# Kernel optimization log

Hardware: AMD Instinct MI355X
Metric: run time of the kernel (lower is better)

The kernel has to match this reference:

```python
import jax, jax.numpy as jnp
import numpy as np
import math

EMBED_DIM = 1024
NUM_HEADS = 16
HEAD_DIM = EMBED_DIM // NUM_HEADS
MAX_LEN = 5000
LN_EPS = 1e-5


def _positional_encoding(max_len, embed_dim):
    pos = np.arange(max_len, dtype=np.float32)[:, None]
    div = np.exp(np.arange(0, embed_dim, 2, dtype=np.float32) * (-math.log(10000.0) / embed_dim))
    pe = np.zeros((max_len, embed_dim), dtype=np.float32)
    pe[:, 0::2] = np.sin(pos * div)
    pe[:, 1::2] = np.cos(pos * div)
    return jnp.asarray(pe)[None]  # [1, max_len, D]


def setup_inputs() -> dict:
    key = jax.random.key(0)
    ks = jax.random.split(key, 12)
    s = 1.0 / math.sqrt(EMBED_DIM)
    D = EMBED_DIM
    return {
        "x": jax.random.normal(ks[0], (4, 2048, D), dtype=jnp.float32),
        "wq": jax.random.uniform(ks[1], (D, D), jnp.float32, -s, s),
        "bq": jax.random.uniform(ks[2], (D,), jnp.float32, -s, s),
        "wk": jax.random.uniform(ks[3], (D, D), jnp.float32, -s, s),
        "bk": jax.random.uniform(ks[4], (D,), jnp.float32, -s, s),
        "wv": jax.random.uniform(ks[5], (D, D), jnp.float32, -s, s),
        "bv": jax.random.uniform(ks[6], (D,), jnp.float32, -s, s),
        "wo": jax.random.uniform(ks[7], (D, D), jnp.float32, -s, s),
        "bo": jax.random.uniform(ks[8], (D,), jnp.float32, -s, s),
        "gamma": jnp.ones((D,), jnp.float32),
        "beta": jnp.zeros((D,), jnp.float32),
        "pe": _positional_encoding(MAX_LEN, D),
    }


def reference(x, wq, bq, wk, bk, wv, bv, wo, bo, gamma, beta, pe):
    B, S, D = x.shape
    H, Hd = NUM_HEADS, HEAD_DIM
    x = x + pe[:, :S, :]
    # projections; weights stored as [in, out]
    q = (x @ wq + bq).reshape(B, S, H, Hd).transpose(0, 2, 1, 3)
    k = (x @ wk + bk).reshape(B, S, H, Hd).transpose(0, 2, 1, 3)
    v = (x @ wv + bv).reshape(B, S, H, Hd).transpose(0, 2, 1, 3)
    scores = jnp.einsum("bhqd,bhkd->bhqk", q, k) / math.sqrt(Hd)
    attn = jax.nn.softmax(scores, axis=-1)  # dropout is identity in eval
    out = jnp.einsum("bhqk,bhkd->bhqd", attn, v)
    out = out.transpose(0, 2, 1, 3).reshape(B, S, D)
    out = out @ wo + bo
    # residual + layernorm
    h = out + x
    mu = jnp.mean(h, axis=-1, keepdims=True)
    var = jnp.var(h, axis=-1, keepdims=True)
    return (h - mu) * jax.lax.rsqrt(var + LN_EPS) * gamma + beta
```

## Files before the change

kernel.cpp:

```cpp
#include <hip/hip_runtime.h>

#define DEV __device__ __forceinline__

typedef __attribute__((ext_vector_type(4))) float floatx4;
typedef __attribute__((ext_vector_type(8))) short short8;

DEV unsigned short f2bf(float f) {
  unsigned u = __float_as_uint(f);
  u += 0x7FFF + ((u >> 16) & 1);
  return (unsigned short)(u >> 16);
}
DEV float bf2f(unsigned short h) { return __uint_as_float(((unsigned)h) << 16); }

DEV unsigned pkbf(float lo, float hi) {
  return __builtin_amdgcn_perm(__float_as_uint(hi) + 0x8000u,
                               __float_as_uint(lo) + 0x8000u, 0x07060302u);
}

#if __has_builtin(__builtin_amdgcn_exp2f)
#define EXP2(x) __builtin_amdgcn_exp2f(x)
#else
#define EXP2(x) exp2f(x)
#endif

#define GLD16(g, l)                                                            \
  __builtin_amdgcn_global_load_lds(                                            \
      (const __attribute__((address_space(1))) void*)(g),                      \
      (__attribute__((address_space(3))) void*)(l), 16, 0, 0)

__global__ void k_wt(const float* __restrict__ w0, const float* __restrict__ w1,
                     const float* __restrict__ w2, const float* __restrict__ w3,
                     unsigned short* __restrict__ wt) {
  __shared__ float t[64][65];
  const float* wsel = (blockIdx.z == 0) ? w0
                    : (blockIdx.z == 1) ? w1
                    : (blockIdx.z == 2) ? w2 : w3;
  unsigned short* out = wt + (size_t)blockIdx.z * 1024 * 1024;
  const int tx = threadIdx.x, ty = threadIdx.y;
  const int k0 = blockIdx.x * 64, n0 = blockIdx.y * 64;
  for (int i = ty; i < 64; i += 4)
    t[i][tx] = wsel[(size_t)(k0 + i) * 1024 + n0 + tx];
  __syncthreads();
  for (int i = ty; i < 64; i += 4)
    out[(size_t)(n0 + i) * 1024 + k0 + tx] = f2bf(t[tx][i]);
}

__global__ void k_addpe(const float* __restrict__ x, const float* __restrict__ pe,
                        float* __restrict__ xf, unsigned short* __restrict__ xb) {
  const int idx = blockIdx.x * 256 + threadIdx.x;
  const int row = idx >> 8;
  const int c4 = idx & 255;
  const int s = row & 2047;
  const float4 xv = ((const float4*)x)[idx];
  const float4 pv = ((const float4*)pe)[s * 256 + c4];
  float4 r;
  r.x = xv.x + pv.x; r.y = xv.y + pv.y; r.z = xv.z + pv.z; r.w = xv.w + pv.w;
  ((float4*)xf)[idx] = r;
  ushort4 o;
  o.x = f2bf(r.x); o.y = f2bf(r.y); o.z = f2bf(r.z); o.w = f2bf(r.w);
  ((ushort4*)xb)[idx] = o;
}

__global__ __launch_bounds__(256) void k_gemmqkv(
    const unsigned short* __restrict__ A, const unsigned short* __restrict__ Bt,
    const float* __restrict__ bqp, const float* __restrict__ bkp,
    const float* __restrict__ bvp, unsigned short* __restrict__ qb,
    unsigned short* __restrict__ kb, unsigned short* __restrict__ vtb) {
  __shared__ unsigned short As[128 * 32];
  __shared__ unsigned short Bs[128 * 32];
  const int tid = threadIdx.x;
  const int lane = tid & 63, wave = tid >> 6;
  const int quad = lane >> 4, l16 = lane & 15;
  const int wm = wave >> 1, wn = wave & 1;
  const int rb = blockIdx.x * 128, cb = blockIdx.y * 128;
  const int which = cb >> 10;
  const float* bias = (which == 0) ? bqp : (which == 1) ? bkp : bvp;
  unsigned short* out = (which == 0) ? qb : (which == 1) ? kb : vtb;

  floatx4 acc[4][4];
  const floatx4 vzero = {0.f, 0.f, 0.f, 0.f};
#pragma unroll
  for (int i = 0; i < 4; ++i)
#pragma unroll
    for (int j = 0; j < 4; ++j) acc[i][j] = vzero;

  for (int k0 = 0; k0 < 1024; k0 += 32) {
#pragma unroll
    for (int r = 0; r < 2; ++r) {
      const int c = r * 256 + tid;
      const int arow = c >> 2, koff = (c & 3) << 3;
      GLD16(A + (size_t)(rb + arow) * 1024 + k0 + koff,
            As + (size_t)(r * 256 + wave * 64) * 8);
      GLD16(Bt + (size_t)(cb + arow) * 1024 + k0 + koff,
            Bs + (size_t)(r * 256 + wave * 64) * 8);
    }
    __syncthreads();
    short8 fa[4], fb[4];
#pragma unroll
    for (int i = 0; i < 4; ++i) {
      fa[i] = *(const short8*)(As + (wm * 64 + i * 16 + l16) * 32 + quad * 8);
      fb[i] = *(const short8*)(Bs + (wn * 64 + i * 16 + l16) * 32 + quad * 8);
    }
#pragma unroll
    for (int mi = 0; mi < 4; ++mi)
#pragma unroll
      for (int ni = 0; ni < 4; ++ni)
        acc[mi][ni] =
            __builtin_amdgcn_mfma_f32_16x16x32_bf16(fa[mi], fb[ni], acc[mi][ni], 0, 0, 0);
    __syncthreads();
  }

#pragma unroll
  for (int ni = 0; ni < 4; ++ni) {
    const int col = cb + wn * 64 + ni * 16 + l16;
    const int cl = col & 1023;
    const float bvv = bias[cl];
    const int h = cl >> 6, d = cl & 63;
#pragma unroll
    for (int mi = 0; mi < 4; ++mi) {
#pragma unroll
      for (int r = 0; r < 4; ++r) {
        const int row = rb + wm * 64 + mi * 16 + quad * 4 + r;
        const int b = row >> 11, s = row & 2047;
        const float val = acc[mi][ni][r] + bvv;
        if (which < 2) {
          out[((size_t)(b * 16 + h) * 2048 + s) * 64 + d] = f2bf(val);
        } else {
          out[((size_t)(b * 16 + h) * 64 + d) * 2048 + s] = f2bf(val);
        }
      }
    }
  }
}

__global__ __launch_bounds__(256) void k_gemmo(
    const unsigned short* __restrict__ A, const unsigned short* __restrict__ Bt,
    const float* __restrict__ bias, unsigned short* __restrict__ out) {
  __shared__ unsigned short As[128 * 32];
  __shared__ unsigned short Bs[128 * 32];
  const int tid = threadIdx.x;
  const int lane = tid & 63, wave = tid >> 6;
  const int quad = lane >> 4, l16 = lane & 15;
  const int wm = wave >> 1, wn = wave & 1;
  const int rb = blockIdx.x * 128, cb = blockIdx.y * 128;

  floatx4 acc[4][4];
  const floatx4 vzero = {0.f, 0.f, 0.f, 0.f};
#pragma unroll
  for (int i = 0; i < 4; ++i)
#pragma unroll
    for (int j = 0; j < 4; ++j) acc[i][j] = vzero;

  for (int k0 = 0; k0 < 1024; k0 += 32) {
#pragma unroll
    for (int r = 0; r < 2; ++r) {
      const int c = r * 256 + tid;
      const int arow = c >> 2, koff = (c & 3) << 3;
      GLD16(A + (size_t)(rb + arow) * 1024 + k0 + koff,
            As + (size_t)(r * 256 + wave * 64) * 8);
      GLD16(Bt + (size_t)(cb + arow) * 1024 + k0 + koff,
            Bs + (size_t)(r * 256 + wave * 64) * 8);
    }
    __syncthreads();
    short8 fa[4], fb[4];
#pragma unroll
    for (int i = 0; i < 4; ++i) {
      fa[i] = *(const short8*)(As + (wm * 64 + i * 16 + l16) * 32 + quad * 8);
      fb[i] = *(const short8*)(Bs + (wn * 64 + i * 16 + l16) * 32 + quad * 8);
    }
#pragma unroll
    for (int mi = 0; mi < 4; ++mi)
#pragma unroll
      for (int ni = 0; ni < 4; ++ni)
        acc[mi][ni] =
            __builtin_amdgcn_mfma_f32_16x16x32_bf16(fa[mi], fb[ni], acc[mi][ni], 0, 0, 0);
    __syncthreads();
  }

#pragma unroll
  for (int ni = 0; ni < 4; ++ni) {
    const int col = cb + wn * 64 + ni * 16 + l16;
    const float bvv = bias[col];
#pragma unroll
    for (int mi = 0; mi < 4; ++mi) {
#pragma unroll
      for (int r = 0; r < 4; ++r) {
        const int row = rb + wm * 64 + mi * 16 + quad * 4 + r;
        out[(size_t)row * 1024 + col] = f2bf(acc[mi][ni][r] + bvv);
      }
    }
  }
}

__global__ __launch_bounds__(256) void k_flash(
    const unsigned short* __restrict__ Q, const unsigned short* __restrict__ Kb,
    const unsigned short* __restrict__ Vt, unsigned short* __restrict__ AO) {
  __shared__ unsigned short Ks[2][64 * 64];
  __shared__ unsigned short Vs[2][64 * 64];
  __shared__ unsigned short Ps[4][32 * 72];
  const int tid = threadIdx.x, lane = tid & 63, wave = tid >> 6;
  const int quad = lane >> 4, l16 = lane & 15;
  const int g = blockIdx.x;
  const int li = g >> 3;
  const int bh = (g & 7) * 8 + (li >> 4);
  const int qt = li & 15;
  const int b = bh >> 4, h = bh & 15;

  const unsigned short* Kh = Kb + (size_t)bh * 2048 * 64;
  const unsigned short* Vh = Vt + (size_t)bh * 64 * 2048;

  const float LAMBDA = 0.125f * 1.4426950408889634f;
  short8 aq[2][2];
  {
    const unsigned short* Qb = Q + ((size_t)bh * 2048 + qt * 128 + wave * 32) * 64;
#pragma unroll
    for (int qi = 0; qi < 2; ++qi)
#pragma unroll
      for (int c = 0; c < 2; ++c) {
        const short8 raw =
            *(const short8*)(Qb + (size_t)(qi * 16 + l16) * 64 + c * 32 + quad * 8);
        short8 sv;
#pragma unroll
        for (int j = 0; j < 8; ++j)
          sv[j] = (short)f2bf(bf2f((unsigned short)raw[j]) * LAMBDA);
        aq[qi][c] = sv;
      }
  }

  const floatx4 vzero = {0.f, 0.f, 0.f, 0.f};
  floatx4 o[2][4];
#pragma unroll
  for (int qi = 0; qi < 2; ++qi)
#pragma unroll
    for (int di = 0; di < 4; ++di) o[qi][di] = vzero;
  float l_p[2] = {0.f, 0.f};
  unsigned short* Pw = Ps[wave];

#define STAGE(ktile, buf)                                                      \
  {                                                                            \
    _Pragma("unroll") for (int r = 0; r < 2; ++r) {                            \
      const int c = r * 256 + tid;                                             \
      const int rw = c >> 3;                                                   \
      const int gc = ((c & 7) ^ (rw & 7)) * 8;                                 \
      GLD16(Kh + (size_t)((ktile) * 64 + rw) * 64 + gc,                        \
            &Ks[buf][(size_t)(r * 256 + wave * 64) * 8]);                      \
      GLD16(Vh + (size_t)rw * 2048 + (ktile) * 64 + gc,                        \
            &Vs[buf][(size_t)(r * 256 + wave * 64) * 8]);                      \
    }                                                                          \
  }

  STAGE(0, 0);
  __syncthreads();

  for (int kt = 0; kt < 32; ++kt) {
    const int buf = kt & 1;
    if (kt + 1 < 32) STAGE(kt + 1, buf ^ 1);

    short8 fk[4][2];
#pragma unroll
    for (int ni = 0; ni < 4; ++ni)
#pragma unroll
      for (int c = 0; c < 2; ++c)
        fk[ni][c] = *(const short8*)(&Ks[buf][(ni * 16 + l16) * 64 +
                                              (((c * 4 + quad) ^ (l16 & 7)) << 3)]);

#pragma unroll
    for (int qi = 0; qi < 2; ++qi) {
      floatx4 p[4];
#pragma unroll
      for (int ni = 0; ni < 4; ++ni) {
        floatx4 t = vzero;
#pragma unroll
        for (int c = 0; c < 2; ++c)
          t = __builtin_amdgcn_mfma_f32_16x16x32_bf16(fk[ni][c], aq[qi][c], t, 0, 0, 0);
        p[ni] = t;
      }
#pragma unroll
      for (int ni = 0; ni < 4; ++ni)
#pragma unroll
        for (int r = 0; r < 4; ++r) p[ni][r] = EXP2(p[ni][r]);
      const float s0 = (p[0][0] + p[0][1]) + (p[0][2] + p[0][3]);
      const float s1 = (p[1][0] + p[1][1]) + (p[1][2] + p[1][3]);
      const float s2 = (p[2][0] + p[2][1]) + (p[2][2] + p[2][3]);
      const float s3 = (p[3][0] + p[3][1]) + (p[3][2] + p[3][3]);
      l_p[qi] += (s0 + s1) + (s2 + s3);
#pragma unroll
      for (int ni = 0; ni < 4; ++ni) {
        uint2 pk;
        pk.x = pkbf(p[ni][0], p[ni][1]);
        pk.y = pkbf(p[ni][2], p[ni][3]);
        *(uint2*)(&Pw[(qi * 16 + l16) * 72 + ni * 16 + quad * 4]) = pk;
      }
    }
    asm volatile("s_waitcnt lgkmcnt(0)" ::: "memory");

#pragma unroll
    for (int c = 0; c < 2; ++c) {
      short8 ap[2];
#pragma unroll
      for (int qi = 0; qi < 2; ++qi)
        ap[qi] = *(const short8*)(&Pw[(qi * 16 + l16) * 72 + c * 32 + quad * 8]);
#pragma unroll
      for (int di = 0; di < 4; ++di) {
        const short8 fv = *(const short8*)(&Vs[buf][(di * 16 + l16) * 64 +
                                                    (((c * 4 + quad) ^ (l16 & 7)) << 3)]);
#pragma unroll
        for (int qi = 0; qi < 2; ++qi)
          o[qi][di] = __builtin_amdgcn_mfma_f32_16x16x32_bf16(ap[qi], fv, o[qi][di], 0, 0, 0);
      }
    }
    __syncthreads();
  }

  float* Al = (float*)Pw;
#pragma unroll
  for (int qi = 0; qi < 2; ++qi) {
    float l = l_p[qi];
    l += __shfl_xor(l, 16);
    l += __shfl_xor(l, 32);
    if (quad == 0) Al[qi * 16 + l16] = 1.0f / l;
  }
  asm volatile("s_waitcnt lgkmcnt(0)" ::: "memory");
#pragma unroll
  for (int qi = 0; qi < 2; ++qi) {
    const floatx4 invl = *(const floatx4*)(&Al[qi * 16 + quad * 4]);
#pragma unroll
    for (int di = 0; di < 4; ++di) {
#pragma unroll
      for (int r = 0; r < 4; ++r) {
        const int s = qt * 128 + wave * 32 + qi * 16 + quad * 4 + r;
        const int col = h * 64 + di * 16 + l16;
        AO[((size_t)b * 2048 + s) * 1024 + col] = f2bf(o[qi][di][r] * invl[r]);
      }
    }
  }
#undef STAGE
}

__global__ __launch_bounds__(256) void k_ln(
    const unsigned short* __restrict__ proj, const float* __restrict__ xpe,
    const float* __restrict__ gamma, const float* __restrict__ beta,
    float* __restrict__ out) {
  const int row = blockIdx.x, tid = threadIdx.x;
  const int lane = tid & 63, wave = tid >> 6;
  const float4 xv = ((const float4*)(xpe + (size_t)row * 1024))[tid];
  const ushort4 pv = ((const ushort4*)(proj + (size_t)row * 1024))[tid];
  const float h0 = xv.x + bf2f(pv.x);
  const float h1 = xv.y + bf2f(pv.y);
  const float h2 = xv.z + bf2f(pv.z);
  const float h3 = xv.w + bf2f(pv.w);
  float s = h0 + h1 + h2 + h3;
  float s2 = h0 * h0 + h1 * h1 + h2 * h2 + h3 * h3;
#pragma unroll
  for (int m = 1; m < 64; m <<= 1) {
    s += __shfl_xor(s, m);
    s2 += __shfl_xor(s2, m);
  }
  __shared__ float rs[4], rq[4];
  if (lane == 0) { rs[wave] = s; rq[wave] = s2; }
  __syncthreads();
  s = rs[0] + rs[1] + rs[2] + rs[3];
  s2 = rq[0] + rq[1] + rq[2] + rq[3];
  const float mu = s * (1.f / 1024.f);
  const float var = s2 * (1.f / 1024.f) - mu * mu;
  const float rstd = rsqrtf(var + 1e-5f);
  const float4 gv = ((const float4*)gamma)[tid];
  const float4 bvv = ((const float4*)beta)[tid];
  float4 ov;
  ov.x = (h0 - mu) * rstd * gv.x + bvv.x;
  ov.y = (h1 - mu) * rstd * gv.y + bvv.y;
  ov.z = (h2 - mu) * rstd * gv.z + bvv.z;
  ov.w = (h3 - mu) * rstd * gv.w + bvv.w;
  ((float4*)(out + (size_t)row * 1024))[tid] = ov;
}

extern "C" void kernel_launch(void* const* d_in, const int* in_sizes, int n_in,
                              void* d_out, int out_size, void* d_ws, size_t ws_size,
                              hipStream_t stream) {
  const float* x = (const float*)d_in[0];
  const float* wq = (const float*)d_in[1];
  const float* bq = (const float*)d_in[2];
  const float* wk = (const float*)d_in[3];
  const float* bk = (const float*)d_in[4];
  const float* wv = (const float*)d_in[5];
  const float* bv = (const float*)d_in[6];
  const float* wo = (const float*)d_in[7];
  const float* bo = (const float*)d_in[8];
  const float* gamma = (const float*)d_in[9];
  const float* beta = (const float*)d_in[10];
  const float* pe = (const float*)d_in[11];

  if (ws_size < 125829120) return;

  char* w = (char*)d_ws;
  unsigned short* wt = (unsigned short*)(w);
  float* xpef = (float*)(w + 8388608);
  unsigned short* xpeb = (unsigned short*)(w + 41943040);
  unsigned short* qb = (unsigned short*)(w + 58720256);
  unsigned short* kb = (unsigned short*)(w + 75497472);
  unsigned short* vtb = (unsigned short*)(w + 92274688);
  unsigned short* aob = (unsigned short*)(w + 109051904);
  unsigned short* projb = qb;

  k_wt<<<dim3(16, 16, 4), dim3(64, 4), 0, stream>>>(wq, wk, wv, wo, wt);
  k_addpe<<<8192, 256, 0, stream>>>(x, pe, xpef, xpeb);
  k_gemmqkv<<<dim3(64, 24), 256, 0, stream>>>(xpeb, wt, bq, bk, bv, qb, kb, vtb);
  k_flash<<<1024, 256, 0, stream>>>(qb, kb, vtb, aob);
  k_gemmo<<<dim3(64, 8), 256, 0, stream>>>(aob, wt + 3145728, bo, projb);
  k_ln<<<8192, 256, 0, stream>>>(projb, xpef, gamma, beta, (float*)d_out);
}
```

Baseline: 354.3 us.

## Split V projection into transposed GEMM, single-buffer flash tiles, MFMA row sums

The V projection moves into its own GEMM that computes W_v^T·X^T, so the transposed V output is written along contiguous sequence positions instead of with a 2048-element stride. The flash kernel drops K/V double buffering in favour of a single buffer with two barriers per tile and a launch bound of 4 blocks, trading load/compute overlap for lower LDS use and higher occupancy. The softmax denominator is now computed with an extra MFMA against a ones vector, using the bf16-rounded probabilities, which removes the scalar sums and the cross-lane reduction.

```diff
diff --git a/kernel.cpp b/kernel.cpp
--- a/kernel.cpp
+++ b/kernel.cpp
@@ -61,11 +61,10 @@
   ((ushort4*)xb)[idx] = o;
 }
 
-__global__ __launch_bounds__(256) void k_gemmqkv(
+__global__ __launch_bounds__(256) void k_gemmqk(
     const unsigned short* __restrict__ A, const unsigned short* __restrict__ Bt,
     const float* __restrict__ bqp, const float* __restrict__ bkp,
-    const float* __restrict__ bvp, unsigned short* __restrict__ qb,
-    unsigned short* __restrict__ kb, unsigned short* __restrict__ vtb) {
+    unsigned short* __restrict__ qb, unsigned short* __restrict__ kb) {
   __shared__ unsigned short As[128 * 32];
   __shared__ unsigned short Bs[128 * 32];
   const int tid = threadIdx.x;
@@ -74,8 +73,8 @@
   const int wm = wave >> 1, wn = wave & 1;
   const int rb = blockIdx.x * 128, cb = blockIdx.y * 128;
   const int which = cb >> 10;
-  const float* bias = (which == 0) ? bqp : (which == 1) ? bkp : bvp;
-  unsigned short* out = (which == 0) ? qb : (which == 1) ? kb : vtb;
+  const float* bias = (which == 0) ? bqp : bkp;
+  unsigned short* out = (which == 0) ? qb : kb;
 
   floatx4 acc[4][4];
   const floatx4 vzero = {0.f, 0.f, 0.f, 0.f};
@@ -122,12 +121,67 @@
       for (int r = 0; r < 4; ++r) {
         const int row = rb + wm * 64 + mi * 16 + quad * 4 + r;
         const int b = row >> 11, s = row & 2047;
-        const float val = acc[mi][ni][r] + bvv;
-        if (which < 2) {
-          out[((size_t)(b * 16 + h) * 2048 + s) * 64 + d] = f2bf(val);
-        } else {
-          out[((size_t)(b * 16 + h) * 64 + d) * 2048 + s] = f2bf(val);
-        }
+        out[((size_t)(b * 16 + h) * 2048 + s) * 64 + d] = f2bf(acc[mi][ni][r] + bvv);
+      }
+    }
+  }
+}
+
+__global__ __launch_bounds__(256) void k_gemmvt(
+    const unsigned short* __restrict__ Av, const unsigned short* __restrict__ Bx,
+    const float* __restrict__ bias, unsigned short* __restrict__ out) {
+  __shared__ unsigned short As[128 * 32];
+  __shared__ unsigned short Bs[128 * 32];
+  const int tid = threadIdx.x;
+  const int lane = tid & 63, wave = tid >> 6;
+  const int quad = lane >> 4, l16 = lane & 15;
+  const int wm = wave >> 1, wn = wave & 1;
+  const int rb = blockIdx.x * 128, cb = blockIdx.y * 128;
+
+  floatx4 acc[4][4];
+  const floatx4 vzero = {0.f, 0.f, 0.f, 0.f};
+#pragma unroll
+  for (int i = 0; i < 4; ++i)
+#pragma unroll
+    for (int j = 0; j < 4; ++j) acc[i][j] = vzero;
+
+  for (int k0 = 0; k0 < 1024; k0 += 32) {
+#pragma unroll
+    for (int r = 0; r < 2; ++r) {
+      const int c = r * 256 + tid;
+      const int arow = c >> 2, koff = (c & 3) << 3;
+      GLD16(Av + (size_t)(rb + arow) * 1024 + k0 + koff,
+            As + (size_t)(r * 256 + wave * 64) * 8);
+      GLD16(Bx + (size_t)(cb + arow) * 1024 + k0 + koff,
+            Bs + (size_t)(r * 256 + wave * 64) * 8);
+    }
+    __syncthreads();
+    short8 fa[4], fb[4];
+#pragma unroll
+    for (int i = 0; i < 4; ++i) {
+      fa[i] = *(const short8*)(As + (wm * 64 + i * 16 + l16) * 32 + quad * 8);
+      fb[i] = *(const short8*)(Bs + (wn * 64 + i * 16 + l16) * 32 + quad * 8);
+    }
+#pragma unroll
+    for (int mi = 0; mi < 4; ++mi)
+#pragma unroll
+      for (int ni = 0; ni < 4; ++ni)
+        acc[mi][ni] =
+            __builtin_amdgcn_mfma_f32_16x16x32_bf16(fa[mi], fb[ni], acc[mi][ni], 0, 0, 0);
+    __syncthreads();
+  }
+
+#pragma unroll
+  for (int mi = 0; mi < 4; ++mi) {
+#pragma unroll
+    for (int r = 0; r < 4; ++r) {
+      const int row = rb + wm * 64 + mi * 16 + quad * 4 + r;
+      const float bvv = bias[row];
+#pragma unroll
+      for (int ni = 0; ni < 4; ++ni) {
+        const int col = cb + wn * 64 + ni * 16 + l16;
+        out[((size_t)(col >> 11) * 1024 + row) * 2048 + (col & 2047)] =
+            f2bf(acc[mi][ni][r] + bvv);
       }
     }
   }
@@ -192,11 +246,11 @@
   }
 }
 
-__global__ __launch_bounds__(256) void k_flash(
+__global__ __launch_bounds__(256, 4) void k_flash(
     const unsigned short* __restrict__ Q, const unsigned short* __restrict__ Kb,
     const unsigned short* __restrict__ Vt, unsigned short* __restrict__ AO) {
-  __shared__ unsigned short Ks[2][64 * 64];
-  __shared__ unsigned short Vs[2][64 * 64];
+  __shared__ unsigned short Ks[64 * 64];
+  __shared__ unsigned short Vs[64 * 64];
   __shared__ unsigned short Ps[4][32 * 72];
   const int tid = threadIdx.x, lane = tid & 63, wave = tid >> 6;
   const int quad = lane >> 4, l16 = lane & 15;
@@ -227,42 +281,43 @@
       }
   }
 
+  short8 onesv;
+#pragma unroll
+  for (int j = 0; j < 8; ++j) onesv[j] = (short)0x3F80;
+
   const floatx4 vzero = {0.f, 0.f, 0.f, 0.f};
   floatx4 o[2][4];
 #pragma unroll
   for (int qi = 0; qi < 2; ++qi)
 #pragma unroll
     for (int di = 0; di < 4; ++di) o[qi][di] = vzero;
-  float l_p[2] = {0.f, 0.f};
+  floatx4 lacc[2] = {vzero, vzero};
   unsigned short* Pw = Ps[wave];
 
-#define STAGE(ktile, buf)                                                      \
+#define STAGE(ktile)                                                           \
   {                                                                            \
     _Pragma("unroll") for (int r = 0; r < 2; ++r) {                            \
       const int c = r * 256 + tid;                                             \
       const int rw = c >> 3;                                                   \
       const int gc = ((c & 7) ^ (rw & 7)) * 8;                                 \
       GLD16(Kh + (size_t)((ktile) * 64 + rw) * 64 + gc,                        \
-            &Ks[buf][(size_t)(r * 256 + wave * 64) * 8]);                      \
+            &Ks[(size_t)(r * 256 + wave * 64) * 8]);                           \
       GLD16(Vh + (size_t)rw * 2048 + (ktile) * 64 + gc,                        \
-            &Vs[buf][(size_t)(r * 256 + wave * 64) * 8]);                      \
+            &Vs[(size_t)(r * 256 + wave * 64) * 8]);                           \
     }                                                                          \
   }
 
-  STAGE(0, 0);
+  STAGE(0);
   __syncthreads();
 
   for (int kt = 0; kt < 32; ++kt) {
-    const int buf = kt & 1;
-    if (kt + 1 < 32) STAGE(kt + 1, buf ^ 1);
-
     short8 fk[4][2];
 #pragma unroll
     for (int ni = 0; ni < 4; ++ni)
 #pragma unroll
       for (int c = 0; c < 2; ++c)
-        fk[ni][c] = *(const short8*)(&Ks[buf][(ni * 16 + l16) * 64 +
-                                              (((c * 4 + quad) ^ (l16 & 7)) << 3)]);
+        fk[ni][c] = *(const short8*)(&Ks[(ni * 16 + l16) * 64 +
+                                         (((c * 4 + quad) ^ (l16 & 7)) << 3)]);
 
 #pragma unroll
     for (int qi = 0; qi < 2; ++qi) {
@@ -279,11 +334,6 @@
       for (int ni = 0; ni < 4; ++ni)
 #pragma unroll
         for (int r = 0; r < 4; ++r) p[ni][r] = EXP2(p[ni][r]);
-      const float s0 = (p[0][0] + p[0][1]) + (p[0][2] + p[0][3]);
-      const float s1 = (p[1][0] + p[1][1]) + (p[1][2] + p[1][3]);
-      const float s2 = (p[2][0] + p[2][1]) + (p[2][2] + p[2][3]);
-      const float s3 = (p[3][0] + p[3][1]) + (p[3][2] + p[3][3]);
-      l_p[qi] += (s0 + s1) + (s2 + s3);
 #pragma unroll
       for (int ni = 0; ni < 4; ++ni) {
         uint2 pk;
@@ -301,29 +351,27 @@
       for (int qi = 0; qi < 2; ++qi)
         ap[qi] = *(const short8*)(&Pw[(qi * 16 + l16) * 72 + c * 32 + quad * 8]);
 #pragma unroll
+      for (int qi = 0; qi < 2; ++qi)
+        lacc[qi] = __builtin_amdgcn_mfma_f32_16x16x32_bf16(ap[qi], onesv, lacc[qi], 0, 0, 0);
+#pragma unroll
       for (int di = 0; di < 4; ++di) {
-        const short8 fv = *(const short8*)(&Vs[buf][(di * 16 + l16) * 64 +
-                                                    (((c * 4 + quad) ^ (l16 & 7)) << 3)]);
+        const short8 fv = *(const short8*)(&Vs[(di * 16 + l16) * 64 +
+                                               (((c * 4 + quad) ^ (l16 & 7)) << 3)]);
 #pragma unroll
         for (int qi = 0; qi < 2; ++qi)
           o[qi][di] = __builtin_amdgcn_mfma_f32_16x16x32_bf16(ap[qi], fv, o[qi][di], 0, 0, 0);
       }
     }
     __syncthreads();
-  }
-
-  float* Al = (float*)Pw;
+    if (kt + 1 < 32) STAGE(kt + 1);
+    __syncthreads();
+  }
+
 #pragma unroll
   for (int qi = 0; qi < 2; ++qi) {
-    float l = l_p[qi];
-    l += __shfl_xor(l, 16);
-    l += __shfl_xor(l, 32);
-    if (quad == 0) Al[qi * 16 + l16] = 1.0f / l;
-  }
-  asm volatile("s_waitcnt lgkmcnt(0)" ::: "memory");
-#pragma unroll
-  for (int qi = 0; qi < 2; ++qi) {
-    const floatx4 invl = *(const floatx4*)(&Al[qi * 16 + quad * 4]);
+    float invl[4];
+#pragma unroll
+    for (int r = 0; r < 4; ++r) invl[r] = __builtin_amdgcn_rcpf(lacc[qi][r]);
 #pragma unroll
     for (int di = 0; di < 4; ++di) {
 #pragma unroll
@@ -404,7 +452,8 @@
 
   k_wt<<<dim3(16, 16, 4), dim3(64, 4), 0, stream>>>(wq, wk, wv, wo, wt);
   k_addpe<<<8192, 256, 0, stream>>>(x, pe, xpef, xpeb);
-  k_gemmqkv<<<dim3(64, 24), 256, 0, stream>>>(xpeb, wt, bq, bk, bv, qb, kb, vtb);
+  k_gemmqk<<<dim3(64, 16), 256, 0, stream>>>(xpeb, wt, bq, bk, qb, kb);
+  k_gemmvt<<<dim3(8, 64), 256, 0, stream>>>(wt + 2097152, xpeb, bv, vtb);
   k_flash<<<1024, 256, 0, stream>>>(qb, kb, vtb, aob);
   k_gemmo<<<dim3(64, 8), 256, 0, stream>>>(aob, wt + 3145728, bo, projb);
   k_ln<<<8192, 256, 0, stream>>>(projb, xpef, gamma, beta, (float*)d_out);
```

Result: faster. 334.7 us (-5.6%).
